# Kernel optimization log

Hardware: AMD Instinct MI355X
Metric: run time of the kernel (lower is better)

## Reference

```python
import jax, jax.numpy as jnp
import numpy as np

B, T1, T2 = 16, 2048, 512
N_MEL, N_TEXT, N_ATT = 80, 256, 256
TEMPERATURE = 0.0005


def _conv1d(x, w, b):
    # x: (B, T, Cin), w: (K, Cin, Cout), 'same' padding
    pad = (w.shape[0] - 1) // 2
    y = jax.lax.conv_general_dilated(
        x, w, window_strides=(1,), padding=[(pad, pad)],
        dimension_numbers=("NWC", "WIO", "NWC"))
    return y + b


def setup_inputs() -> dict:
    key = jax.random.key(0)
    ks = jax.random.split(key, 16)
    s = 0.05
    queries = jax.random.normal(ks[0], (B, N_MEL, T1), jnp.float32)
    keys = jax.random.normal(ks[1], (B, T2, N_TEXT), jnp.float32)
    attn_prior = jax.random.uniform(ks[2], (B, T2, T1), jnp.float32)
    lengths = jax.random.randint(ks[3], (B,), T2 // 2, T2 + 1)
    mask = jnp.arange(T2)[None, :] >= lengths[:, None]  # True = padding
    # key_proj params: Conv(256->512,k3), ReLU, Conv(512->256,k1)
    kw1 = jax.random.normal(ks[4], (3, N_TEXT, 2 * N_TEXT), jnp.float32) * s
    kb1 = jnp.zeros((2 * N_TEXT,), jnp.float32)
    kw2 = jax.random.normal(ks[5], (1, 2 * N_TEXT, N_ATT), jnp.float32) * s
    kb2 = jnp.zeros((N_ATT,), jnp.float32)
    # query_proj params: Conv(80->160,k3), ReLU, Conv(160->80,k1), ReLU, Conv(80->256,k1)
    qw1 = jax.random.normal(ks[6], (3, N_MEL, 2 * N_MEL), jnp.float32) * s
    qb1 = jnp.zeros((2 * N_MEL,), jnp.float32)
    qw2 = jax.random.normal(ks[7], (1, 2 * N_MEL, N_MEL), jnp.float32) * s
    qb2 = jnp.zeros((N_MEL,), jnp.float32)
    qw3 = jax.random.normal(ks[8], (1, N_MEL, N_ATT), jnp.float32) * s
    qb3 = jnp.zeros((N_ATT,), jnp.float32)
    return dict(queries=queries, keys=keys, mask=mask, attn_prior=attn_prior,
                kw1=kw1, kb1=kb1, kw2=kw2, kb2=kb2,
                qw1=qw1, qb1=qb1, qw2=qw2, qb2=qb2, qw3=qw3, qb3=qb3)


def reference(queries, keys, mask, attn_prior,
              kw1, kb1, kw2, kb2, qw1, qb1, qw2, qb2, qw3, qb3):
    # keys: (B, T2, C_text) -> ke: (B, T2, n_att)
    ke = _conv1d(jax.nn.relu(_conv1d(keys, kw1, kb1)), kw2, kb2)
    # queries: (B, C_mel, T1) -> (B, T1, C_mel) -> qe: (B, T1, n_att)
    q = queries.transpose(0, 2, 1)
    q = jax.nn.relu(_conv1d(jax.nn.relu(_conv1d(q, qw1, qb1)), qw2, qb2))
    qe = _conv1d(q, qw3, qb3)
    # pairwise squared L2 distance over channels, via |q|^2 + |k|^2 - 2 q.k
    q2 = jnp.sum(qe * qe, axis=-1)            # (B, T1)
    k2 = jnp.sum(ke * ke, axis=-1)            # (B, T2)
    qk = jnp.einsum("btc,bsc->bts", qe, ke)   # (B, T1, T2)
    dist = q2[:, :, None] + k2[:, None, :] - 2.0 * qk
    attn = (-TEMPERATURE * dist)[:, None]      # (B, 1, T1, T2)
    # prior in log-space
    attn = jax.nn.log_softmax(attn, axis=3) + jnp.log(
        attn_prior.transpose(0, 2, 1)[:, None] + 1e-8)
    attn_logprob = attn
    attn = jnp.where(mask[:, None, None, :], -jnp.inf, attn)
    attn = jax.nn.softmax(attn, axis=3)
    return attn, attn_logprob
```

## Files before the change

kernel.cpp:

```cpp
#include <hip/hip_runtime.h>
#include <cmath>

#define NB    16
#define TT1   2048
#define TT2   512
#define NATT  256
#define TEMP  0.0005f

#define KP_SZ   (NB*514*256)
#define KE_SZ   (NB*512*256)
#define QP_SZ   (NB*2050*80)
#define QE_SZ   (NB*2048*256)
#define W1T_SZ  (512*768)
#define W2T_SZ  (256*512)
#define W3T_SZ  (160*256)
#define W4T_SZ  (80*160)
#define W5T_SZ  (256*96)
#define WTOT_SZ (W1T_SZ+W2T_SZ+W3T_SZ+W4T_SZ+W5T_SZ)
#define LGP_SZ  (NB*TT1*TT2)

#define PREP_PLT_BLK  ((TT1/64)*(TT2/64)*NB)
#define PREP_PK_BLK   (KP_SZ/256)
#define PREP_WT_BLK   (WTOT_SZ/256)
#define PREP_QT_BLK   (NB*(TT1/64))
#define CONV_KEY_BLK  (NB*512/32)
#define CONV_QRY_BLK  (NB*2048/128)

typedef __attribute__((ext_vector_type(8))) short short8v;
typedef __attribute__((ext_vector_type(4))) float f32x4;

__device__ inline ushort f2bf(float f) {
    unsigned int u = __float_as_uint(f);
    u += 0x7fff + ((u >> 16) & 1);
    return (ushort)(u >> 16);
}
__device__ inline float bf2f(ushort u) {
    return __uint_as_float(((unsigned int)u) << 16);
}


__global__ __launch_bounds__(256) void prep_kernel(
    const float* __restrict__ keys, ushort* __restrict__ kp,
    const float* __restrict__ kw1, const float* __restrict__ kw2,
    const float* __restrict__ qw1, const float* __restrict__ qw2,
    const float* __restrict__ qw3,
    ushort* __restrict__ w1t, ushort* __restrict__ w2t, ushort* __restrict__ w3t,
    ushort* __restrict__ w4t, ushort* __restrict__ w5t,
    const float* __restrict__ queries, ushort* __restrict__ qp,
    const float* __restrict__ prior, ushort* __restrict__ lgp)
{
    __shared__ float T[80][65];
    const int bx  = blockIdx.x;
    const int tid = threadIdx.x;

    if (bx < PREP_PLT_BLK) {
        const int l    = bx;
        const int t1_0 = (l & 31) * 64;
        const int t2_0 = ((l >> 5) & 7) * 64;
        const int b    = l >> 8;
        const int j  = tid & 63;
        const int i0 = (tid >> 6) * 16;
        #pragma unroll
        for (int r = 0; r < 16; ++r)
            T[i0 + r][j] = __builtin_nontemporal_load(
                prior + ((size_t)b * TT2 + t2_0 + i0 + r) * TT1 + t1_0 + j);
        __syncthreads();
        #pragma unroll
        for (int r = 0; r < 16; ++r) {
            const int p = i0 + r;
            const float v = T[j][p];
            lgp[((size_t)b * TT1 + t1_0 + p) * TT2 + t2_0 + j] = f2bf(__logf(v + 1e-8f));
        }
        return;
    }
    if (bx < PREP_PLT_BLK + PREP_PK_BLK) {
        const int idx = (bx - PREP_PLT_BLK) * 256 + tid;
        int c = idx & 255;
        int r = (idx >> 8) % 514;
        int b = idx / (514 * 256);
        float v = 0.f;
        if (r >= 1 && r <= 512)
            v = keys[((size_t)b * 512 + (r - 1)) * 256 + c];
        kp[idx] = f2bf(v);
        return;
    }
    if (bx < PREP_PLT_BLK + PREP_PK_BLK + PREP_WT_BLK) {
        int idx = (bx - PREP_PLT_BLK - PREP_PK_BLK) * 256 + tid;
        const float* w; ushort* wt; int Kreal, Kpad, N;
        if (idx < W1T_SZ) {
            w = kw1; wt = w1t; Kreal = 768; Kpad = 768; N = 512;
        } else if ((idx -= W1T_SZ) < W2T_SZ) {
            w = kw2; wt = w2t; Kreal = 512; Kpad = 512; N = 256;
        } else if ((idx -= W2T_SZ) < W3T_SZ) {
            w = qw1; wt = w3t; Kreal = 240; Kpad = 256; N = 160;
        } else if ((idx -= W3T_SZ) < W4T_SZ) {
            w = qw2; wt = w4t; Kreal = 160; Kpad = 160; N = 80;
        } else {
            idx -= W4T_SZ;
            w = qw3; wt = w5t; Kreal = 80; Kpad = 96; N = 256;
        }
        int k = idx % Kpad;
        int n = idx / Kpad;
        wt[idx] = (k < Kreal) ? f2bf(w[(size_t)k * N + n]) : (ushort)0;
        return;
    }
    {
        const int l  = bx - PREP_PLT_BLK - PREP_PK_BLK - PREP_WT_BLK;
        const int b  = l >> 5;
        const int t0 = (l & 31) * 64;
        const int g  = tid >> 6;
        const int j  = tid & 63;
        #pragma unroll
        for (int r = 0; r < 20; ++r) {
            const int c = g * 20 + r;
            T[c][j] = queries[((size_t)b * 80 + c) * 2048 + t0 + j];
        }
        __syncthreads();
        const int tt = tid >> 2;
        const int c0 = (tid & 3) * 20;
        ushort* qrow = qp + (size_t)b * (2050 * 80) + (size_t)(t0 + tt + 1) * 80 + c0;
        #pragma unroll
        for (int i4 = 0; i4 < 5; ++i4) {
            ushort4 st;
            st.x = f2bf(T[c0 + i4 * 4 + 0][tt]);
            st.y = f2bf(T[c0 + i4 * 4 + 1][tt]);
            st.z = f2bf(T[c0 + i4 * 4 + 2][tt]);
            st.w = f2bf(T[c0 + i4 * 4 + 3][tt]);
            *(ushort4*)(qrow + i4 * 4) = st;
        }
        if (t0 == 0 && tid < 80)
            qp[(size_t)b * (2050 * 80) + tid] = 0;
        if (t0 == 2048 - 64 && tid < 80)
            qp[(size_t)b * (2050 * 80) + (size_t)2049 * 80 + tid] = 0;
    }
}


__global__ __launch_bounds__(512, 4) void conv_kernel(
    const ushort* __restrict__ kp, const ushort* __restrict__ w1t,
    const float* __restrict__ kb1, const ushort* __restrict__ w2t,
    const float* __restrict__ kb2, ushort* __restrict__ ke, float* __restrict__ k2,
    const ushort* __restrict__ qp, const ushort* __restrict__ w3t,
    const float* __restrict__ qb1, const ushort* __restrict__ w4t,
    const float* __restrict__ qb2, const ushort* __restrict__ w5t,
    const float* __restrict__ qb3, ushort* __restrict__ qe)
{
    __shared__ __align__(16) unsigned char smem[69632];
    const int bx   = blockIdx.x;
    const int tid  = threadIdx.x;
    const int wv   = tid >> 6;
    const int lane = tid & 63;
    const int lr   = lane & 15;
    const int lk   = lane >> 4;

    if (bx < CONV_KEY_BLK) {
        ushort (*h1s)[536] = (ushort(*)[536])smem;
        float (*k2part)[8] = (float(*)[8])(smem + 32 * 536 * 2);
        const int m0 = bx * 32;

        {
            const ushort* arow0;
            const ushort* arow1;
            {
                const int m = m0 + lr;
                arow0 = kp + (size_t)(m >> 9) * (514 * 256) + (size_t)(m & 511) * 256 + lk * 8;
                const int m1 = m0 + 16 + lr;
                arow1 = kp + (size_t)(m1 >> 9) * (514 * 256) + (size_t)(m1 & 511) * 256 + lk * 8;
            }
            const ushort* wtb = w1t + (size_t)(wv * 64 + lr) * 768 + lk * 8;
            f32x4 acc[2][4];
            #pragma unroll
            for (int mf = 0; mf < 2; ++mf)
                #pragma unroll
                for (int f = 0; f < 4; ++f) acc[mf][f] = (f32x4){0.f, 0.f, 0.f, 0.f};

            short8v a0 = *(const short8v*)(arow0);
            short8v a1 = *(const short8v*)(arow1);
            short8v b0 = *(const short8v*)(wtb);
            short8v b1 = *(const short8v*)(wtb + (size_t)1 * 16 * 768);
            short8v b2 = *(const short8v*)(wtb + (size_t)2 * 16 * 768);
            short8v b3 = *(const short8v*)(wtb + (size_t)3 * 16 * 768);
            #pragma unroll
            for (int ks = 0; ks < 24; ++ks) {
                short8v na0, na1, nb0, nb1, nb2, nb3;
                if (ks < 23) {
                    const int o = (ks + 1) * 32;
                    na0 = *(const short8v*)(arow0 + o);
                    na1 = *(const short8v*)(arow1 + o);
                    nb0 = *(const short8v*)(wtb + o);
                    nb1 = *(const short8v*)(wtb + (size_t)1 * 16 * 768 + o);
                    nb2 = *(const short8v*)(wtb + (size_t)2 * 16 * 768 + o);
                    nb3 = *(const short8v*)(wtb + (size_t)3 * 16 * 768 + o);
                }
                acc[0][0] = __builtin_amdgcn_mfma_f32_16x16x32_bf16(a0, b0, acc[0][0], 0, 0, 0);
                acc[1][0] = __builtin_amdgcn_mfma_f32_16x16x32_bf16(a1, b0, acc[1][0], 0, 0, 0);
                acc[0][1] = __builtin_amdgcn_mfma_f32_16x16x32_bf16(a0, b1, acc[0][1], 0, 0, 0);
                acc[1][1] = __builtin_amdgcn_mfma_f32_16x16x32_bf16(a1, b1, acc[1][1], 0, 0, 0);
                acc[0][2] = __builtin_amdgcn_mfma_f32_16x16x32_bf16(a0, b2, acc[0][2], 0, 0, 0);
                acc[1][2] = __builtin_amdgcn_mfma_f32_16x16x32_bf16(a1, b2, acc[1][2], 0, 0, 0);
                acc[0][3] = __builtin_amdgcn_mfma_f32_16x16x32_bf16(a0, b3, acc[0][3], 0, 0, 0);
                acc[1][3] = __builtin_amdgcn_mfma_f32_16x16x32_bf16(a1, b3, acc[1][3], 0, 0, 0);
                if (ks < 23) {
                    a0 = na0; a1 = na1; b0 = nb0; b1 = nb1; b2 = nb2; b3 = nb3;
                }
            }
            const short8v bb[4] = {b0, b1, b2, b3};
            (void)bb;
            #pragma unroll
            for (int f = 0; f < 4; ++f) {
                const int col = wv * 64 + f * 16 + lr;
                const float bv = kb1[col];
                #pragma unroll
                for (int mf = 0; mf < 2; ++mf)
                    #pragma unroll
                    for (int r = 0; r < 4; ++r)
                        h1s[mf * 16 + lk * 4 + r][col] = f2bf(fmaxf(acc[mf][f][r] + bv, 0.f));
            }
        }
        __syncthreads();

        {
            f32x4 acc[2][2];
            #pragma unroll
            for (int mf = 0; mf < 2; ++mf)
                #pragma unroll
                for (int f = 0; f < 2; ++f) acc[mf][f] = (f32x4){0.f, 0.f, 0.f, 0.f};
            const ushort* w2b = w2t + (size_t)(wv * 32 + lr) * 512 + lk * 8;
            short8v b0 = *(const short8v*)(w2b);
            short8v b1 = *(const short8v*)(w2b + (size_t)16 * 512);
            #pragma unroll
            for (int ks = 0; ks < 16; ++ks) {
                short8v nb0, nb1;
                if (ks < 15) {
                    const int o = (ks + 1) * 32;
                    nb0 = *(const short8v*)(w2b + o);
                    nb1 = *(const short8v*)(w2b + (size_t)16 * 512 + o);
                }
                const short8v a0 = *(const short8v*)&h1s[lr][lk * 8 + ks * 32];
                const short8v a1 = *(const short8v*)&h1s[16 + lr][lk * 8 + ks * 32];
                acc[0][0] = __builtin_amdgcn_mfma_f32_16x16x32_bf16(a0, b0, acc[0][0], 0, 0, 0);
                acc[1][0] = __builtin_amdgcn_mfma_f32_16x16x32_bf16(a1, b0, acc[1][0], 0, 0, 0);
                acc[0][1] = __builtin_amdgcn_mfma_f32_16x16x32_bf16(a0, b1, acc[0][1], 0, 0, 0);
                acc[1][1] = __builtin_amdgcn_mfma_f32_16x16x32_bf16(a1, b1, acc[1][1], 0, 0, 0);
                if (ks < 15) { b0 = nb0; b1 = nb1; }
            }
            float ss[2][4];
            #pragma unroll
            for (int mf = 0; mf < 2; ++mf)
                #pragma unroll
                for (int r = 0; r < 4; ++r) ss[mf][r] = 0.f;
            #pragma unroll
            for (int f = 0; f < 2; ++f) {
                const int col = wv * 32 + f * 16 + lr;
                const float bv = kb2[col];
                #pragma unroll
                for (int mf = 0; mf < 2; ++mf)
                    #pragma unroll
                    for (int r = 0; r < 4; ++r) {
                        const float o = acc[mf][f][r] + bv;
                        ke[(size_t)(m0 + mf * 16 + lk * 4 + r) * 256 + col] = f2bf(o);
                        ss[mf][r] += o * o;
                    }
            }
            #pragma unroll
            for (int mf = 0; mf < 2; ++mf)
                #pragma unroll
                for (int r = 0; r < 4; ++r) {
                    #pragma unroll
                    for (int off = 1; off < 16; off <<= 1)
                        ss[mf][r] += __shfl_xor(ss[mf][r], off);
                }
            if (lr == 0) {
                #pragma unroll
                for (int mf = 0; mf < 2; ++mf)
                    #pragma unroll
                    for (int r = 0; r < 4; ++r)
                        k2part[mf * 16 + lk * 4 + r][wv] = ss[mf][r];
            }
        }
        __syncthreads();
        if (tid < 32) {
            float s = 0.f;
            #pragma unroll
            for (int w = 0; w < 8; ++w) s += k2part[tid][w];
            k2[m0 + tid] = -TEMP * s;
        }
        return;
    }
    {
        ushort (*s1)[168] = (ushort(*)[168])smem;
        ushort (*s2)[104] = (ushort(*)[104])(smem + 128 * 168 * 2);
        const int m0 = (bx - CONV_KEY_BLK) * 128;
        const int cg = wv >> 2;
        const int rb = (wv & 3) * 32;

        #pragma unroll
        for (int i = 0; i < 4; ++i) {
            const int e = tid * 4 + i;
            s2[e >> 4][80 + (e & 15)] = 0;
        }

        {
            const ushort* arow0;
            const ushort* arow1;
            {
                const int m = m0 + rb + lr;
                arow0 = qp + (size_t)(m >> 11) * (2050 * 80) + (size_t)(m & 2047) * 80 + lk * 8;
                const int m1 = m0 + rb + 16 + lr;
                arow1 = qp + (size_t)(m1 >> 11) * (2050 * 80) + (size_t)(m1 & 2047) * 80 + lk * 8;
            }
            const ushort* w3b = w3t + (size_t)(cg * 5 * 16 + lr) * 256 + lk * 8;
            f32x4 acc[2][5];
            #pragma unroll
            for (int mf = 0; mf < 2; ++mf)
                #pragma unroll
                for (int f = 0; f < 5; ++f) acc[mf][f] = (f32x4){0.f, 0.f, 0.f, 0.f};

            short8v a0 = *(const short8v*)(arow0);
            short8v a1 = *(const short8v*)(arow1);
            short8v bq[5];
            #pragma unroll
            for (int f = 0; f < 5; ++f)
                bq[f] = *(const short8v*)(w3b + (size_t)f * 16 * 256);
            #pragma unroll
            for (int ks = 0; ks < 8; ++ks) {
                short8v na0, na1, nb[5];
                if (ks < 7) {
                    const int o = (ks + 1) * 32;
                    na0 = *(const short8v*)(arow0 + o);
                    na1 = *(const short8v*)(arow1 + o);
                    #pragma unroll
                    for (int f = 0; f < 5; ++f)
                        nb[f] = *(const short8v*)(w3b + (size_t)f * 16 * 256 + o);
                }
                #pragma unroll
                for (int f = 0; f < 5; ++f) {
                    acc[0][f] = __builtin_amdgcn_mfma_f32_16x16x32_bf16(a0, bq[f], acc[0][f], 0, 0, 0);
                    acc[1][f] = __builtin_amdgcn_mfma_f32_16x16x32_bf16(a1, bq[f], acc[1][f], 0, 0, 0);
                }
                if (ks < 7) {
                    a0 = na0; a1 = na1;
                    #pragma unroll
                    for (int f = 0; f < 5; ++f) bq[f] = nb[f];
                }
            }
            #pragma unroll
            for (int f = 0; f < 5; ++f) {
                const int col = (cg * 5 + f) * 16 + lr;
                const float bv = qb1[col];
                #pragma unroll
                for (int mf = 0; mf < 2; ++mf)
                    #pragma unroll
                    for (int r = 0; r < 4; ++r)
                        s1[rb + mf * 16 + lk * 4 + r][col] = f2bf(fmaxf(acc[mf][f][r] + bv, 0.f));
            }
        }
        __syncthreads();

        {
            const int nf = cg ? 2 : 3;
            const int f0 = cg ? 3 : 0;
            f32x4 acc[2][3];
            #pragma unroll
            for (int mf = 0; mf < 2; ++mf)
                #pragma unroll
                for (int f = 0; f < 3; ++f) acc[mf][f] = (f32x4){0.f, 0.f, 0.f, 0.f};
            #pragma unroll
            for (int ks = 0; ks < 5; ++ks) {
                const short8v a0 = *(const short8v*)&s1[rb + lr][lk * 8 + ks * 32];
                const short8v a1 = *(const short8v*)&s1[rb + 16 + lr][lk * 8 + ks * 32];
                #pragma unroll
                for (int f = 0; f < 3; ++f) {
                    if (f < nf) {
                        const short8v b = *(const short8v*)(w4t + (size_t)((f0 + f) * 16 + lr) * 160
                                                                + lk * 8 + ks * 32);
                        acc[0][f] = __builtin_amdgcn_mfma_f32_16x16x32_bf16(a0, b, acc[0][f], 0, 0, 0);
                        acc[1][f] = __builtin_amdgcn_mfma_f32_16x16x32_bf16(a1, b, acc[1][f], 0, 0, 0);
                    }
                }
            }
            #pragma unroll
            for (int f = 0; f < 3; ++f) {
                if (f < nf) {
                    const int col = (f0 + f) * 16 + lr;
                    const float bv = qb2[col];
                    #pragma unroll
                    for (int mf = 0; mf < 2; ++mf)
                        #pragma unroll
                        for (int r = 0; r < 4; ++r)
                            s2[rb + mf * 16 + lk * 4 + r][col] = f2bf(fmaxf(acc[mf][f][r] + bv, 0.f));
                }
            }
        }
        __syncthreads();

        {
            f32x4 acc[2][8];
            #pragma unroll
            for (int mf = 0; mf < 2; ++mf)
                #pragma unroll
                for (int f = 0; f < 8; ++f) acc[mf][f] = (f32x4){0.f, 0.f, 0.f, 0.f};
            #pragma unroll
            for (int ks = 0; ks < 3; ++ks) {
                const short8v a0 = *(const short8v*)&s2[rb + lr][lk * 8 + ks * 32];
                const short8v a1 = *(const short8v*)&s2[rb + 16 + lr][lk * 8 + ks * 32];
                #pragma unroll
                for (int f = 0; f < 8; ++f) {
                    const short8v b = *(const short8v*)(w5t + (size_t)((cg * 8 + f) * 16 + lr) * 96
                                                            + lk * 8 + ks * 32);
                    acc[0][f] = __builtin_amdgcn_mfma_f32_16x16x32_bf16(a0, b, acc[0][f], 0, 0, 0);
                    acc[1][f] = __builtin_amdgcn_mfma_f32_16x16x32_bf16(a1, b, acc[1][f], 0, 0, 0);
                }
            }
            #pragma unroll
            for (int f = 0; f < 8; ++f) {
                const int col = (cg * 8 + f) * 16 + lr;
                const float bv = qb3[col];
                #pragma unroll
                for (int mf = 0; mf < 2; ++mf)
                    #pragma unroll
                    for (int r = 0; r < 4; ++r)
                        qe[(size_t)(m0 + rb + mf * 16 + lk * 4 + r) * 256 + col] = f2bf(acc[mf][f][r] + bv);
            }
        }
    }
}


__global__ __launch_bounds__(512) void attn_kernel(
    const ushort* __restrict__ qe, const ushort* __restrict__ ke,
    const float* __restrict__ k2t, const ushort* __restrict__ lgp,
    const unsigned char* __restrict__ mask,
    float* __restrict__ out_attn, float* __restrict__ out_lp)
{
    __shared__ float S[16][516];
    __shared__ float rowZ[16];
    __shared__ float rowM[16];
    __shared__ float rowI[16];
    const int b    = blockIdx.x >> 7;
    const int t1_0 = (blockIdx.x & 127) << 4;
    const int tid  = threadIdx.x;
    const int lane = tid & 63;
    const int wv   = tid >> 6;
    const int t2   = tid;

    const bool mv = mask[(size_t)b * TT2 + t2] != 0;
    ushort lg[16];
    #pragma unroll
    for (int r = 0; r < 16; ++r)
        lg[r] = lgp[((size_t)b * TT1 + t1_0 + r) * TT2 + t2];

    {
        const int lr = lane & 15;
        const int lk = lane >> 4;
        const ushort* qrow = qe + ((size_t)b * TT1 + t1_0 + lr) * NATT + lk * 8;
        short8v a[8];
        #pragma unroll
        for (int k = 0; k < 8; ++k)
            a[k] = *(const short8v*)(qrow + k * 32);

        const ushort* kbase = ke + ((size_t)b * TT2 + wv * 64 + lr) * NATT + lk * 8;
        #pragma unroll
        for (int n = 0; n < 4; ++n) {
            f32x4 acc = {0.f, 0.f, 0.f, 0.f};
            const ushort* kb = kbase + (size_t)n * 16 * NATT;
            #pragma unroll
            for (int k = 0; k < 8; ++k) {
                short8v bfr = *(const short8v*)(kb + k * 32);
                acc = __builtin_amdgcn_mfma_f32_16x16x32_bf16(a[k], bfr, acc, 0, 0, 0);
            }
            const int col = wv * 64 + n * 16 + lr;
            const float k2v = k2t[(size_t)b * TT2 + col];
            #pragma unroll
            for (int r = 0; r < 4; ++r)
                S[lk * 4 + r][col] = fmaf(2.0f * TEMP, acc[r], k2v);
        }
    }
    __syncthreads();

    const int rr = tid >> 5;
    const int jj = tid & 31;

    {
        float sv[16];
        #pragma unroll
        for (int k = 0; k < 16; ++k) sv[k] = S[rr][jj + 32 * k];
        float mx = sv[0];
        #pragma unroll
        for (int k = 1; k < 16; ++k) mx = fmaxf(mx, sv[k]);
        #pragma unroll
        for (int off = 16; off; off >>= 1) mx = fmaxf(mx, __shfl_xor(mx, off));
        float se = 0.f;
        #pragma unroll
        for (int k = 0; k < 16; ++k) se += __expf(sv[k] - mx);
        #pragma unroll
        for (int off = 16; off; off >>= 1) se += __shfl_xor(se, off);
        if (jj == 0) rowZ[rr] = mx + __logf(se);
    }
    __syncthreads();

    #pragma unroll
    for (int r = 0; r < 16; ++r) {
        const float uu = S[r][t2] + bf2f(lg[r]);
        out_lp[((size_t)b * TT1 + t1_0 + r) * TT2 + t2] = uu - rowZ[r];
        S[r][t2] = mv ? -INFINITY : uu;
    }
    __syncthreads();

    {
        float uv[16];
        #pragma unroll
        for (int k = 0; k < 16; ++k) uv[k] = S[rr][jj + 32 * k];
        float mx = uv[0];
        #pragma unroll
        for (int k = 1; k < 16; ++k) mx = fmaxf(mx, uv[k]);
        #pragma unroll
        for (int off = 16; off; off >>= 1) mx = fmaxf(mx, __shfl_xor(mx, off));
        float se = 0.f;
        #pragma unroll
        for (int k = 0; k < 16; ++k) se += __expf(uv[k] - mx);
        #pragma unroll
        for (int off = 16; off; off >>= 1) se += __shfl_xor(se, off);
        if (jj == 0) { rowM[rr] = mx; rowI[rr] = 1.0f / se; }
    }
    __syncthreads();

    #pragma unroll
    for (int r = 0; r < 16; ++r) {
        const float a = __expf(S[r][t2] - rowM[r]) * rowI[r];
        out_attn[((size_t)b * TT1 + t1_0 + r) * TT2 + t2] = a;
    }
}


extern "C" void kernel_launch(void* const* d_in, const int* in_sizes, int n_in,
                              void* d_out, int out_size, void* d_ws, size_t ws_size,
                              hipStream_t stream) {
    const float* queries = (const float*)d_in[0];
    const float* keys    = (const float*)d_in[1];
    const unsigned char* mask = (const unsigned char*)d_in[2];
    const float* prior   = (const float*)d_in[3];
    const float* kw1 = (const float*)d_in[4];
    const float* kb1 = (const float*)d_in[5];
    const float* kw2 = (const float*)d_in[6];
    const float* kb2 = (const float*)d_in[7];
    const float* qw1 = (const float*)d_in[8];
    const float* qb1 = (const float*)d_in[9];
    const float* qw2 = (const float*)d_in[10];
    const float* qb2 = (const float*)d_in[11];
    const float* qw3 = (const float*)d_in[12];
    const float* qb3 = (const float*)d_in[13];

    ushort* us   = (ushort*)d_ws;
    ushort* kp   = us;
    ushort* ke   = kp  + KP_SZ;
    ushort* qp   = ke  + KE_SZ;
    ushort* qe   = qp  + QP_SZ;
    ushort* w1t  = qe  + QE_SZ;
    ushort* w2t  = w1t + W1T_SZ;
    ushort* w3t  = w2t + W2T_SZ;
    ushort* w4t  = w3t + W3T_SZ;
    ushort* w5t  = w4t + W4T_SZ;
    ushort* lgp  = w5t + W5T_SZ;
    float*  k2   = (float*)(lgp + LGP_SZ);

    float* out_attn = (float*)d_out;
    float* out_lp   = out_attn + (size_t)NB * TT1 * TT2;

    prep_kernel<<<PREP_PLT_BLK + PREP_PK_BLK + PREP_WT_BLK + PREP_QT_BLK, 256, 0, stream>>>(
        keys, kp, kw1, kw2, qw1, qw2, qw3, w1t, w2t, w3t, w4t, w5t,
        queries, qp, prior, lgp);

    conv_kernel<<<CONV_KEY_BLK + CONV_QRY_BLK, 512, 0, stream>>>(
        kp, w1t, kb1, w2t, kb2, ke, k2,
        qp, w3t, qb1, w4t, qb2, w5t, qb3, qe);

    attn_kernel<<<NB * (TT1 / 16), 512, 0, stream>>>(
        qe, ke, k2, lgp, mask, out_attn, out_lp);
}
```

Measured before the change: 172.4 us.

## Keep softmax rows in registers and vectorize prior log-transpose loads

Result: no change. 173.3 us (+0.6%).

```diff
diff --git a/kernel.cpp b/kernel.cpp
--- a/kernel.cpp
+++ b/kernel.cpp
@@ -58,13 +58,21 @@
         const int t1_0 = (l & 31) * 64;
         const int t2_0 = ((l >> 5) & 7) * 64;
         const int b    = l >> 8;
+        const int j4 = tid & 15;
+        const int r0 = tid >> 4;
+        #pragma unroll
+        for (int p = 0; p < 4; ++p) {
+            const f32x4 v = __builtin_nontemporal_load(
+                (const f32x4*)(prior + ((size_t)b * TT2 + t2_0 + r0 + p * 16) * TT1
+                                + t1_0 + j4 * 4));
+            T[r0 + p * 16][j4 * 4 + 0] = v.x;
+            T[r0 + p * 16][j4 * 4 + 1] = v.y;
+            T[r0 + p * 16][j4 * 4 + 2] = v.z;
+            T[r0 + p * 16][j4 * 4 + 3] = v.w;
+        }
+        __syncthreads();
         const int j  = tid & 63;
         const int i0 = (tid >> 6) * 16;
-        #pragma unroll
-        for (int r = 0; r < 16; ++r)
-            T[i0 + r][j] = __builtin_nontemporal_load(
-                prior + ((size_t)b * TT2 + t2_0 + i0 + r) * TT1 + t1_0 + j);
-        __syncthreads();
         #pragma unroll
         for (int r = 0; r < 16; ++r) {
             const int p = i0 + r;
@@ -204,8 +212,6 @@
                     a0 = na0; a1 = na1; b0 = nb0; b1 = nb1; b2 = nb2; b3 = nb3;
                 }
             }
-            const short8v bb[4] = {b0, b1, b2, b3};
-            (void)bb;
             #pragma unroll
             for (int f = 0; f < 4; ++f) {
                 const int col = wv * 64 + f * 16 + lr;
@@ -434,21 +440,11 @@
     float* __restrict__ out_attn, float* __restrict__ out_lp)
 {
     __shared__ float S[16][516];
-    __shared__ float rowZ[16];
-    __shared__ float rowM[16];
-    __shared__ float rowI[16];
     const int b    = blockIdx.x >> 7;
     const int t1_0 = (blockIdx.x & 127) << 4;
     const int tid  = threadIdx.x;
     const int lane = tid & 63;
     const int wv   = tid >> 6;
-    const int t2   = tid;
-
-    const bool mv = mask[(size_t)b * TT2 + t2] != 0;
-    ushort lg[16];
-    #pragma unroll
-    for (int r = 0; r < 16; ++r)
-        lg[r] = lgp[((size_t)b * TT1 + t1_0 + r) * TT2 + t2];
 
     {
         const int lr = lane & 15;
@@ -480,55 +476,50 @@
 
     const int rr = tid >> 5;
     const int jj = tid & 31;
-
-    {
-        float sv[16];
-        #pragma unroll
-        for (int k = 0; k < 16; ++k) sv[k] = S[rr][jj + 32 * k];
-        float mx = sv[0];
-        #pragma unroll
-        for (int k = 1; k < 16; ++k) mx = fmaxf(mx, sv[k]);
-        #pragma unroll
-        for (int off = 16; off; off >>= 1) mx = fmaxf(mx, __shfl_xor(mx, off));
-        float se = 0.f;
-        #pragma unroll
-        for (int k = 0; k < 16; ++k) se += __expf(sv[k] - mx);
-        #pragma unroll
-        for (int off = 16; off; off >>= 1) se += __shfl_xor(se, off);
-        if (jj == 0) rowZ[rr] = mx + __logf(se);
-    }
-    __syncthreads();
-
-    #pragma unroll
-    for (int r = 0; r < 16; ++r) {
-        const float uu = S[r][t2] + bf2f(lg[r]);
-        out_lp[((size_t)b * TT1 + t1_0 + r) * TT2 + t2] = uu - rowZ[r];
-        S[r][t2] = mv ? -INFINITY : uu;
-    }
-    __syncthreads();
-
-    {
-        float uv[16];
-        #pragma unroll
-        for (int k = 0; k < 16; ++k) uv[k] = S[rr][jj + 32 * k];
-        float mx = uv[0];
-        #pragma unroll
-        for (int k = 1; k < 16; ++k) mx = fmaxf(mx, uv[k]);
-        #pragma unroll
-        for (int off = 16; off; off >>= 1) mx = fmaxf(mx, __shfl_xor(mx, off));
-        float se = 0.f;
-        #pragma unroll
-        for (int k = 0; k < 16; ++k) se += __expf(uv[k] - mx);
-        #pragma unroll
-        for (int off = 16; off; off >>= 1) se += __shfl_xor(se, off);
-        if (jj == 0) { rowM[rr] = mx; rowI[rr] = 1.0f / se; }
-    }
-    __syncthreads();
-
-    #pragma unroll
-    for (int r = 0; r < 16; ++r) {
-        const float a = __expf(S[r][t2] - rowM[r]) * rowI[r];
-        out_attn[((size_t)b * TT1 + t1_0 + r) * TT2 + t2] = a;
+    const ushort* lgr = lgp + ((size_t)b * TT1 + t1_0 + rr) * TT2 + jj;
+    const unsigned char* mkr = mask + (size_t)b * TT2 + jj;
+
+    float sv[16], uv[16];
+    unsigned int mbits = 0;
+    #pragma unroll
+    for (int k = 0; k < 16; ++k) {
+        sv[k] = S[rr][jj + 32 * k];
+        uv[k] = sv[k] + bf2f(lgr[32 * k]);
+        if (mkr[32 * k]) mbits |= (1u << k);
+    }
+
+    float mx1 = sv[0];
+    #pragma unroll
+    for (int k = 1; k < 16; ++k) mx1 = fmaxf(mx1, sv[k]);
+    #pragma unroll
+    for (int off = 16; off; off >>= 1) mx1 = fmaxf(mx1, __shfl_xor(mx1, off));
+    float se1 = 0.f;
+    #pragma unroll
+    for (int k = 0; k < 16; ++k) se1 += __expf(sv[k] - mx1);
+    #pragma unroll
+    for (int off = 16; off; off >>= 1) se1 += __shfl_xor(se1, off);
+    const float logZ = mx1 + __logf(se1);
+
+    float mx2 = -INFINITY;
+    #pragma unroll
+    for (int k = 0; k < 16; ++k)
+        if (!((mbits >> k) & 1)) mx2 = fmaxf(mx2, uv[k]);
+    #pragma unroll
+    for (int off = 16; off; off >>= 1) mx2 = fmaxf(mx2, __shfl_xor(mx2, off));
+    float se2 = 0.f;
+    #pragma unroll
+    for (int k = 0; k < 16; ++k)
+        se2 += ((mbits >> k) & 1) ? 0.f : __expf(uv[k] - mx2);
+    #pragma unroll
+    for (int off = 16; off; off >>= 1) se2 += __shfl_xor(se2, off);
+    const float inv = 1.0f / se2;
+
+    float* lpr = out_lp   + ((size_t)b * TT1 + t1_0 + rr) * TT2 + jj;
+    float* atr = out_attn + ((size_t)b * TT1 + t1_0 + rr) * TT2 + jj;
+    #pragma unroll
+    for (int k = 0; k < 16; ++k) {
+        lpr[32 * k] = uv[k] - logZ;
+        atr[32 * k] = ((mbits >> k) & 1) ? 0.f : __expf(uv[k] - mx2) * inv;
     }
 }
 
```
